# Optimization experiments

Hardware: AMD Instinct MI355X
Metric: run time of the kernel (lower is better)

## Reference

```python
import jax, jax.numpy as jnp
import numpy as np

BS, N_CTX, N_HEADS, WIDTH = 2, 2048, 8, 32
N_TOK = 512


def setup_inputs() -> dict:
    key = jax.random.key(0)
    kq, kk, kv, ki = jax.random.split(key, 4)
    q = jax.random.normal(kq, (BS, N_CTX, N_HEADS, WIDTH), dtype=jnp.float32)
    k = jax.random.normal(kk, (BS, N_CTX, N_HEADS, WIDTH), dtype=jnp.float32)
    v = jax.random.normal(kv, (BS, N_CTX, N_HEADS, WIDTH), dtype=jnp.float32)
    indx = jnp.sort(jax.random.randint(ki, (N_TOK,), 0, N_CTX, dtype=jnp.int64))
    return {"q": q, "k": k, "v": v, "indx": indx}


def reference(q, k, v, indx):
    # q, k, v: (bs, n_ctx, n_heads, width); indx: (n_tok,) token ids to attend over
    n_tok = indx.shape[0]
    scale = jnp.float32(1.0 / np.sqrt(n_tok))
    qg = q[:, indx]  # (bs, n_tok, h, w) -- gathered tokens (t axis in torch code)
    kg = k[:, indx]  # (bs, n_tok, h, w) -- gathered tokens (s axis in torch code)
    vg = v[:, indx]  # (bs, n_tok, h, w)
    # L1 distance scores: ww[b,s,t,h] = scale * sum_w |q[b,indx[t],h,w] - k[b,indx[s],h,w]|
    diff = jnp.abs(qg[:, None, :, :, :] - kg[:, :, None, :, :])  # (bs, s, t, h, w)
    scores = -scale * jnp.sum(diff, axis=-1)  # (bs, s, t, h)
    attn = jax.nn.softmax(scores, axis=2)  # softmax over t (matches torch softmax(-1) on (b,h,s,t))
    # out[b,s,h,w] = sum_t attn[b,s,t,h] * v[b,indx[t],h,w]
    out = jnp.einsum('bsth,bthw->bshw', attn, vg)
    return out
```

## Files before the change

kernel.cpp:

```cpp
#include <hip/hip_runtime.h>

#define NCTX 2048
#define NH   8
#define WD   32
#define NTOK 512

static constexpr float SCALE = 0.04419417382415922f;

template<int S>
__global__ __launch_bounds__(512, 4) void l1attn_main(
    const float* __restrict__ q, const float* __restrict__ k,
    const float* __restrict__ v, const int* __restrict__ indx,
    float* __restrict__ dst ) {
  constexpr int WIN = NTOK / S;
  __shared__ int   indxS[NTOK];
  __shared__ float ldsQ[WIN * 32];
  __shared__ float ldsV[WIN * 32];
  __shared__ float accS[64 * 33];
  __shared__ float lS[64];

  const int tid  = threadIdx.x;
  const int bid  = blockIdx.x;
  const int pr   = bid / S;
  const int jw   = bid % S;
  const int b    = pr >> 6;
  const int h    = (pr >> 3) & 7;
  const int rg   = pr & 7;

  indxS[tid] = indx[tid];
  for (int i = tid; i < 64 * 33; i += 512) accS[i] = 0.f;
  if (tid < 64) lS[tid] = 0.f;
  __syncthreads();

  const float* qb = q + ((size_t)b * NCTX * NH) * WD + h * WD;
  const float* vb = v + ((size_t)b * NCTX * NH) * WD + h * WD;
  const float* kb = k + ((size_t)b * NCTX * NH) * WD + h * WD;

  for (int i = tid; i < WIN * 8; i += 512) {
    const int t = i >> 3, sg = i & 7;
    const int tok = indxS[jw * WIN + t];
    const float4* qr = (const float4*)(qb + (size_t)tok * (NH * WD));
    const float4* vr = (const float4*)(vb + (size_t)tok * (NH * WD));
    ((float4*)ldsQ)[i] = qr[sg];
    ((float4*)ldsV)[i] = vr[sg];
  }

  const int lane = tid & 63;
  const int wave = __builtin_amdgcn_readfirstlane(tid >> 6);
  float kg[32];
  {
    const int s = rg * 64 + lane;
    const float4* kr = (const float4*)(kb + (size_t)indxS[s] * (NH * WD));
#pragma unroll
    for (int i = 0; i < 8; ++i) {
      float4 t = kr[i];
      kg[4*i+0] = t.x; kg[4*i+1] = t.y; kg[4*i+2] = t.z; kg[4*i+3] = t.w;
    }
  }

  float acc[32];
#pragma unroll
  for (int i = 0; i < 32; ++i) acc[i] = 0.f;
  float l = 0.f;

  __syncthreads();

  constexpr int JPW = WIN / 8;
  const int jloc0 = wave * JPW;
  for (int jj = 0; jj < JPW; ++jj) {
    const float* qrow = ldsQ + (jloc0 + jj) * 32;
    const float* vrow = ldsV + (jloc0 + jj) * 32;

    float d0, d1, d2, d3;
    {
      float4 t = ((const float4*)qrow)[0];
      d0 = fabsf(t.x - kg[0]); d1 = fabsf(t.y - kg[1]);
      d2 = fabsf(t.z - kg[2]); d3 = fabsf(t.w - kg[3]);
    }
#pragma unroll
    for (int i = 1; i < 8; ++i) {
      float4 t = ((const float4*)qrow)[i];
      d0 += fabsf(t.x - kg[4*i+0]);
      d1 += fabsf(t.y - kg[4*i+1]);
      d2 += fabsf(t.z - kg[4*i+2]);
      d3 += fabsf(t.w - kg[4*i+3]);
    }
    const float d = (d0 + d1) + (d2 + d3);
    const float p = __expf(-SCALE * d);
    l += p;
#pragma unroll
    for (int i = 0; i < 8; ++i) {
      float4 t = ((const float4*)vrow)[i];
      acc[4*i+0] = fmaf(p, t.x, acc[4*i+0]);
      acc[4*i+1] = fmaf(p, t.y, acc[4*i+1]);
      acc[4*i+2] = fmaf(p, t.z, acc[4*i+2]);
      acc[4*i+3] = fmaf(p, t.w, acc[4*i+3]);
    }
  }

#pragma unroll
  for (int w = 0; w < 32; ++w) atomicAdd(&accS[lane * 33 + w], acc[w]);
  atomicAdd(&lS[lane], l);
  __syncthreads();

  if (S > 1) {
    float* wsB = dst + (size_t)bid * 2112;
    for (int i = tid; i < 2048; i += 512)
      wsB[i] = accS[(i >> 5) * 33 + (i & 31)];
    if (tid < 64) wsB[2048 + tid] = lS[tid];
  } else {
    for (int i = tid; i < 2048; i += 512) {
      const int r = i >> 5, w = i & 31;
      dst[(((size_t)b * NTOK + rg * 64 + r) * NH + h) * WD + w] =
          accS[r * 33 + w] / lS[r];
    }
  }
}

template<int S>
__global__ __launch_bounds__(1024) void l1attn_combine(
    const float* __restrict__ ws, float* __restrict__ out) {
  const int gid = blockIdx.x * 1024 + threadIdx.x;
  const int w  = gid & 31;
  const int r  = (gid >> 5) & 63;
  const int pr = gid >> 11;
  const float* base = ws + (size_t)pr * S * 2112;
  float a = 0.f, ls = 0.f;
#pragma unroll
  for (int jwi = 0; jwi < S; ++jwi) {
    a  += base[jwi * 2112 + r * 32 + w];
    ls += base[jwi * 2112 + 2048 + r];
  }
  const int b = pr >> 6, h = (pr >> 3) & 7, rg = pr & 7;
  out[(((size_t)b * NTOK + rg * 64 + r) * NH + h) * WD + w] = a / ls;
}

extern "C" void kernel_launch(void* const* d_in, const int* in_sizes, int n_in,
                              void* d_out, int out_size, void* d_ws, size_t ws_size,
                              hipStream_t stream) {
  const float* q    = (const float*)d_in[0];
  const float* k    = (const float*)d_in[1];
  const float* v    = (const float*)d_in[2];
  const int*   indx = (const int*)d_in[3];
  float*       out  = (float*)d_out;

  const size_t need4 = (size_t)512 * 2112 * sizeof(float);
  const size_t need2 = (size_t)256 * 2112 * sizeof(float);
  if (ws_size >= need4) {
    hipLaunchKernelGGL((l1attn_main<4>), dim3(512), dim3(512), 0, stream,
                       q, k, v, indx, (float*)d_ws);
    hipLaunchKernelGGL((l1attn_combine<4>), dim3(256), dim3(1024), 0, stream,
                       (const float*)d_ws, out);
  } else if (ws_size >= need2) {
    hipLaunchKernelGGL((l1attn_main<2>), dim3(256), dim3(512), 0, stream,
                       q, k, v, indx, (float*)d_ws);
    hipLaunchKernelGGL((l1attn_combine<2>), dim3(256), dim3(1024), 0, stream,
                       (const float*)d_ws, out);
  } else {
    hipLaunchKernelGGL((l1attn_main<1>), dim3(128), dim3(512), 0, stream,
                       q, k, v, indx, out);
  }
}
```

Measured before the change: 66.09 us.

## Split width across half-waves, halve row groups, and window Q/V staging

Each wave now splits the 32-wide feature dimension between its two 32-lane halves. Each lane holds 16 K values and 16 accumulators, and the partial L1 distances are combined with a cross-half shuffle. Row groups shrink from 64 to 32 rows, which doubles the block count, and Q/V are staged in fixed 128-token LDS windows with a barrier between windows. The aim is more parallelism, lower register pressure (launch bounds raised to 6 blocks) and less LDS, at the cost of an extra shuffle per score, more blocks that each reload K/Q/V, and extra barriers.

```diff
diff --git a/kernel.cpp b/kernel.cpp
--- a/kernel.cpp
+++ b/kernel.cpp
@@ -8,111 +8,120 @@
 static constexpr float SCALE = 0.04419417382415922f;
 
 template<int S>
-__global__ __launch_bounds__(512, 4) void l1attn_main(
+__global__ __launch_bounds__(512, 6) void l1attn_main(
     const float* __restrict__ q, const float* __restrict__ k,
     const float* __restrict__ v, const int* __restrict__ indx,
     float* __restrict__ dst ) {
-  constexpr int WIN = NTOK / S;
+  constexpr int JSPAN = NTOK / S;
+  constexpr int NWIN  = JSPAN / 128;
   __shared__ int   indxS[NTOK];
-  __shared__ float ldsQ[WIN * 32];
-  __shared__ float ldsV[WIN * 32];
-  __shared__ float accS[64 * 33];
-  __shared__ float lS[64];
+  __shared__ float ldsQ[128 * 32];
+  __shared__ float ldsV[128 * 32];
+  __shared__ float accS[32 * 33];
+  __shared__ float lS[32];
 
-  const int tid  = threadIdx.x;
-  const int bid  = blockIdx.x;
-  const int pr   = bid / S;
-  const int jw   = bid % S;
-  const int b    = pr >> 6;
-  const int h    = (pr >> 3) & 7;
-  const int rg   = pr & 7;
+  const int tid = threadIdx.x;
+  const int bid = blockIdx.x;
+  const int pr  = bid / S;
+  const int jw  = bid % S;
+  const int plane = pr >> 4;
+  const int rg    = pr & 15;
+  const int b     = plane >> 3;
+  const int h     = plane & 7;
 
   indxS[tid] = indx[tid];
-  for (int i = tid; i < 64 * 33; i += 512) accS[i] = 0.f;
-  if (tid < 64) lS[tid] = 0.f;
+  for (int i = tid; i < 32 * 33; i += 512) accS[i] = 0.f;
+  if (tid < 32) lS[tid] = 0.f;
   __syncthreads();
 
   const float* qb = q + ((size_t)b * NCTX * NH) * WD + h * WD;
   const float* vb = v + ((size_t)b * NCTX * NH) * WD + h * WD;
   const float* kb = k + ((size_t)b * NCTX * NH) * WD + h * WD;
 
-  for (int i = tid; i < WIN * 8; i += 512) {
-    const int t = i >> 3, sg = i & 7;
-    const int tok = indxS[jw * WIN + t];
-    const float4* qr = (const float4*)(qb + (size_t)tok * (NH * WD));
-    const float4* vr = (const float4*)(vb + (size_t)tok * (NH * WD));
-    ((float4*)ldsQ)[i] = qr[sg];
-    ((float4*)ldsV)[i] = vr[sg];
-  }
+  const int lane  = tid & 63;
+  const int wave  = __builtin_amdgcn_readfirstlane(tid >> 6);
+  const int r     = lane & 31;
+  const int whalf = lane >> 5;
 
-  const int lane = tid & 63;
-  const int wave = __builtin_amdgcn_readfirstlane(tid >> 6);
-  float kg[32];
+  float kg[16];
   {
-    const int s = rg * 64 + lane;
-    const float4* kr = (const float4*)(kb + (size_t)indxS[s] * (NH * WD));
+    const int s = rg * 32 + r;
+    const float4* kr =
+        (const float4*)(kb + (size_t)indxS[s] * (NH * WD) + whalf * 16);
 #pragma unroll
-    for (int i = 0; i < 8; ++i) {
+    for (int i = 0; i < 4; ++i) {
       float4 t = kr[i];
       kg[4*i+0] = t.x; kg[4*i+1] = t.y; kg[4*i+2] = t.z; kg[4*i+3] = t.w;
     }
   }
 
-  float acc[32];
+  float acc[16];
 #pragma unroll
-  for (int i = 0; i < 32; ++i) acc[i] = 0.f;
+  for (int i = 0; i < 16; ++i) acc[i] = 0.f;
   float l = 0.f;
 
-  __syncthreads();
+  for (int wnd = 0; wnd < NWIN; ++wnd) {
+    if (wnd) __syncthreads();
 
-  constexpr int JPW = WIN / 8;
-  const int jloc0 = wave * JPW;
-  for (int jj = 0; jj < JPW; ++jj) {
-    const float* qrow = ldsQ + (jloc0 + jj) * 32;
-    const float* vrow = ldsV + (jloc0 + jj) * 32;
+    const int tok0 = jw * JSPAN + wnd * 128;
+    for (int i = tid; i < 128 * 8; i += 512) {
+      const int t = i >> 3, sg = i & 7;
+      const int tok = indxS[tok0 + t];
+      ((float4*)ldsQ)[i] = ((const float4*)(qb + (size_t)tok * (NH * WD)))[sg];
+      ((float4*)ldsV)[i] = ((const float4*)(vb + (size_t)tok * (NH * WD)))[sg];
+    }
+    __syncthreads();
 
-    float d0, d1, d2, d3;
-    {
-      float4 t = ((const float4*)qrow)[0];
-      d0 = fabsf(t.x - kg[0]); d1 = fabsf(t.y - kg[1]);
-      d2 = fabsf(t.z - kg[2]); d3 = fabsf(t.w - kg[3]);
-    }
+    const int j0 = wave * 16;
+    for (int jj = 0; jj < 16; ++jj) {
+      const float* qrow = ldsQ + (j0 + jj) * 32 + whalf * 16;
+      const float* vrow = ldsV + (j0 + jj) * 32 + whalf * 16;
+
+      float d0, d1, d2, d3;
+      {
+        float4 t = ((const float4*)qrow)[0];
+        d0 = fabsf(t.x - kg[0]); d1 = fabsf(t.y - kg[1]);
+        d2 = fabsf(t.z - kg[2]); d3 = fabsf(t.w - kg[3]);
+      }
 #pragma unroll
-    for (int i = 1; i < 8; ++i) {
-      float4 t = ((const float4*)qrow)[i];
-      d0 += fabsf(t.x - kg[4*i+0]);
-      d1 += fabsf(t.y - kg[4*i+1]);
-      d2 += fabsf(t.z - kg[4*i+2]);
-      d3 += fabsf(t.w - kg[4*i+3]);
-    }
-    const float d = (d0 + d1) + (d2 + d3);
-    const float p = __expf(-SCALE * d);
-    l += p;
+      for (int i = 1; i < 4; ++i) {
+        float4 t = ((const float4*)qrow)[i];
+        d0 += fabsf(t.x - kg[4*i+0]);
+        d1 += fabsf(t.y - kg[4*i+1]);
+        d2 += fabsf(t.z - kg[4*i+2]);
+        d3 += fabsf(t.w - kg[4*i+3]);
+      }
+      float d = (d0 + d1) + (d2 + d3);
+      d += __shfl_xor(d, 32, 64);
+      const float p = __expf(-SCALE * d);
+      l += p;
 #pragma unroll
-    for (int i = 0; i < 8; ++i) {
-      float4 t = ((const float4*)vrow)[i];
-      acc[4*i+0] = fmaf(p, t.x, acc[4*i+0]);
-      acc[4*i+1] = fmaf(p, t.y, acc[4*i+1]);
-      acc[4*i+2] = fmaf(p, t.z, acc[4*i+2]);
-      acc[4*i+3] = fmaf(p, t.w, acc[4*i+3]);
+      for (int i = 0; i < 4; ++i) {
+        float4 t = ((const float4*)vrow)[i];
+        acc[4*i+0] = fmaf(p, t.x, acc[4*i+0]);
+        acc[4*i+1] = fmaf(p, t.y, acc[4*i+1]);
+        acc[4*i+2] = fmaf(p, t.z, acc[4*i+2]);
+        acc[4*i+3] = fmaf(p, t.w, acc[4*i+3]);
+      }
     }
   }
 
 #pragma unroll
-  for (int w = 0; w < 32; ++w) atomicAdd(&accS[lane * 33 + w], acc[w]);
-  atomicAdd(&lS[lane], l);
+  for (int w = 0; w < 16; ++w)
+    atomicAdd(&accS[r * 33 + whalf * 16 + w], acc[w]);
+  if (whalf == 0) atomicAdd(&lS[r], l);
   __syncthreads();
 
   if (S > 1) {
-    float* wsB = dst + (size_t)bid * 2112;
-    for (int i = tid; i < 2048; i += 512)
+    float* wsB = dst + (size_t)bid * 1056;
+    for (int i = tid; i < 1024; i += 512)
       wsB[i] = accS[(i >> 5) * 33 + (i & 31)];
-    if (tid < 64) wsB[2048 + tid] = lS[tid];
+    if (tid < 32) wsB[1024 + tid] = lS[tid];
   } else {
-    for (int i = tid; i < 2048; i += 512) {
-      const int r = i >> 5, w = i & 31;
-      dst[(((size_t)b * NTOK + rg * 64 + r) * NH + h) * WD + w] =
-          accS[r * 33 + w] / lS[r];
+    for (int i = tid; i < 1024; i += 512) {
+      const int rr = i >> 5, w = i & 31;
+      dst[(((size_t)b * NTOK + rg * 32 + rr) * NH + h) * WD + w] =
+          accS[rr * 33 + w] / lS[rr];
     }
   }
 }
@@ -122,17 +131,18 @@
     const float* __restrict__ ws, float* __restrict__ out) {
   const int gid = blockIdx.x * 1024 + threadIdx.x;
   const int w  = gid & 31;
-  const int r  = (gid >> 5) & 63;
-  const int pr = gid >> 11;
-  const float* base = ws + (size_t)pr * S * 2112;
+  const int r  = (gid >> 5) & 31;
+  const int pr = gid >> 10;
+  const float* base = ws + (size_t)pr * S * 1056;
   float a = 0.f, ls = 0.f;
 #pragma unroll
   for (int jwi = 0; jwi < S; ++jwi) {
-    a  += base[jwi * 2112 + r * 32 + w];
-    ls += base[jwi * 2112 + 2048 + r];
+    a  += base[jwi * 1056 + r * 32 + w];
+    ls += base[jwi * 1056 + 1024 + r];
   }
-  const int b = pr >> 6, h = (pr >> 3) & 7, rg = pr & 7;
-  out[(((size_t)b * NTOK + rg * 64 + r) * NH + h) * WD + w] = a / ls;
+  const int plane = pr >> 4, rg = pr & 15;
+  const int b = plane >> 3, h = plane & 7;
+  out[(((size_t)b * NTOK + rg * 32 + r) * NH + h) * WD + w] = a / ls;
 }
 
 extern "C" void kernel_launch(void* const* d_in, const int* in_sizes, int n_in,
@@ -144,20 +154,20 @@
   const int*   indx = (const int*)d_in[3];
   float*       out  = (float*)d_out;
 
-  const size_t need4 = (size_t)512 * 2112 * sizeof(float);
-  const size_t need2 = (size_t)256 * 2112 * sizeof(float);
+  const size_t need4 = (size_t)1024 * 1056 * sizeof(float);
+  const size_t need2 = (size_t)512  * 1056 * sizeof(float);
   if (ws_size >= need4) {
-    hipLaunchKernelGGL((l1attn_main<4>), dim3(512), dim3(512), 0, stream,
+    hipLaunchKernelGGL((l1attn_main<4>), dim3(1024), dim3(512), 0, stream,
                        q, k, v, indx, (float*)d_ws);
     hipLaunchKernelGGL((l1attn_combine<4>), dim3(256), dim3(1024), 0, stream,
                        (const float*)d_ws, out);
   } else if (ws_size >= need2) {
-    hipLaunchKernelGGL((l1attn_main<2>), dim3(256), dim3(512), 0, stream,
+    hipLaunchKernelGGL((l1attn_main<2>), dim3(512), dim3(512), 0, stream,
                        q, k, v, indx, (float*)d_ws);
     hipLaunchKernelGGL((l1attn_combine<2>), dim3(256), dim3(1024), 0, stream,
                        (const float*)d_ws, out);
   } else {
-    hipLaunchKernelGGL((l1attn_main<1>), dim3(128), dim3(512), 0, stream,
+    hipLaunchKernelGGL((l1attn_main<1>), dim3(256), dim3(512), 0, stream,
                        q, k, v, indx, out);
   }
 }
```

Measured after the change: 64.96 us. About the same (-1.7%).
